# Optimization experiments

Measured on AMD Instinct MI355X. Metric: run time of the kernel, lower is better.

## Reference

```python
import jax, jax.numpy as jnp
import numpy as np

EPS = 1e-6


def _feature_map(x):
    # elu(x) + 1
    return jax.nn.elu(x) + 1.0


def _causal_dot(Qb, Kb, V):
    """Causal linear attention numerator for 3 stacked branches.
    Qb, Kb: [3, N, L, H, D]; V: [N, L, H, Dv] -> out [3, N, L, H, Dv].
    out[b,n,l,h,:] = sum_{s<=l} (Qb[b,n,l,h,:] . Kb[b,n,s,h,:]) V[n,s,h,:]
    computed with an O(L) recurrent scan over cumulative KV outer products.
    """
    Qs = jnp.moveaxis(Qb, 2, 0)  # [L, 3, N, H, D]
    Ks = jnp.moveaxis(Kb, 2, 0)  # [L, 3, N, H, D]
    Vs = jnp.moveaxis(V, 1, 0)   # [L, N, H, Dv]
    B, N, _, H, D = Qb.shape
    Dv = V.shape[-1]
    S0 = jnp.zeros((B, N, H, D, Dv), dtype=Qb.dtype)

    def step(S, inp):
        q, k, v = inp  # q,k: [3,N,H,D], v: [N,H,Dv]
        S = S + k[..., :, None] * v[None, :, :, None, :]
        o = jnp.einsum('bnhi,bnhij->bnhj', q, S)
        return S, o

    _, out = jax.lax.scan(step, S0, (Qs, Ks, Vs))  # out: [L,3,N,H,Dv]
    return jnp.moveaxis(out, 0, 2)  # [3,N,L,H,Dv]


def setup_inputs() -> dict:
    key = jax.random.key(0)
    ks = jax.random.split(key, 5)
    N, L, H, D = 4, 2048, 8, 128
    return {
        'queries': jax.random.normal(ks[0], (N, L, H, D), dtype=jnp.float32),
        'q2': jax.random.normal(ks[1], (N, L, H, D), dtype=jnp.float32),
        'keys': jax.random.normal(ks[2], (N, L, H, D), dtype=jnp.float32),
        'values': jax.random.normal(ks[3], (N, L, H, D), dtype=jnp.float32),
        'key_lengths': jnp.ones((N, L), dtype=jnp.float32),
        'omega': jax.random.normal(ks[4], (H, D, D), dtype=jnp.float32),
    }


def reference(queries, q2, keys, values, key_lengths, omega):
    N, L, H, D = queries.shape
    Q = _feature_map(queries)                       # [N,L,H,D]
    K = _feature_map(keys) * key_lengths[:, :, None, None]

    # Delta[n,l,h,i] = l/L for all n,h,i -> projection through omega reduces to
    # (l/L) * sum_i omega[h,i,j], same math as einsum('nlhi,hij->nlhj', Delta, omega).
    delta = (jnp.arange(L, dtype=queries.dtype) / L)        # [L]
    t = delta[:, None, None] * jnp.sum(omega, axis=1)[None]  # [L,H,D]
    sin_t, cos_t = jnp.sin(t), jnp.cos(t)
    s2, c2, sc = sin_t ** 2, cos_t ** 2, sin_t * cos_t       # [L,H,D] each

    # Q_term = sin(phi(q2))^2 * feature_map(queries)
    q2_proj = jnp.einsum('nlhi,hij->nlhj', q2, omega)
    Q_term = (jnp.sin(q2_proj) ** 2) * Q                     # [N,L,H,D]

    # Branch trig weights: Q gets [sin^2, cos^2, sin*cos], K gets [cos^2, sin^2, sin*cos]
    wq = jnp.stack([s2, c2, sc])[:, None]  # [3,1,L,H,D]
    wk = jnp.stack([c2, s2, sc])[:, None]
    Qb = Q_term[None] * wq                 # [3,N,L,H,D]
    Kb = K[None] * wk                      # [3,N,L,H,D]

    # Denominator terms Z_b = <Q_b[l], cumsum_{s<=l} K_b[s]>
    Kcum = jnp.cumsum(Kb, axis=2)
    Z = jnp.einsum('bnlhi,bnlhi->bnlh', Qb, Kcum)   # [3,N,L,H]

    Vb = _causal_dot(Qb, Kb, values)                # [3,N,L,H,D]

    numerator = Vb[0] + Vb[1] - 2.0 * Vb[2]
    denominator = Z[0] + Z[1] - 2.0 * Z[2] + EPS
    return numerator / denominator[:, :, :, None]
```

## Files before the change

kernel.cpp:

```cpp
#include <hip/hip_runtime.h>


typedef float f32x4 __attribute__((ext_vector_type(4)));
typedef short s16x8 __attribute__((ext_vector_type(8)));
typedef short s16x4 __attribute__((ext_vector_type(4)));
typedef unsigned short u16;

static constexpr int    Ln   = 2048;
static constexpr size_t NHLD = (size_t)32 * 2048 * 128;
static constexpr size_t KSB  = (size_t)32 * 16 * 128;

__device__ __forceinline__ float b2f(u16 s) {
  union { unsigned u; float f; } x; x.u = ((unsigned)s) << 16; return x.f;
}
__device__ __forceinline__ u16 f2b(float f) {
  union { float f; unsigned u; } x; x.f = f;
  unsigned r = x.u + 0x7fffu + ((x.u >> 16) & 1u);
  return (u16)(r >> 16);
}
__device__ __forceinline__ s16x8 pack8(f32x4 a, f32x4 b) {
  s16x8 r;
  r[0] = (short)f2b(a[0]); r[1] = (short)f2b(a[1]); r[2] = (short)f2b(a[2]); r[3] = (short)f2b(a[3]);
  r[4] = (short)f2b(b[0]); r[5] = (short)f2b(b[1]); r[6] = (short)f2b(b[2]); r[7] = (short)f2b(b[3]);
  return r;
}

__global__ __launch_bounds__(256) void k_omega(const float* __restrict__ om,
                                               u16* __restrict__ wt, float* __restrict__ osum) {
  __shared__ alignas(16) u16 T[128][136];
  int h = blockIdx.x, t = threadIdx.x;
  for (int idx = t; idx < 128 * 32; idx += 256) {
    int i = idx >> 5, cs = (idx & 31) << 2;
    f32x4 vv = *(const f32x4*)(om + ((size_t)(h * 128 + i)) * 128 + cs);
    T[i][cs + 0] = f2b(vv[0]); T[i][cs + 1] = f2b(vv[1]);
    T[i][cs + 2] = f2b(vv[2]); T[i][cs + 3] = f2b(vv[3]);
  }
  if (t < 128) {
    float acc = 0.f;
    for (int i = 0; i < 128; i++) acc += om[((size_t)(h * 128 + i)) * 128 + t];
    osum[h * 128 + t] = acc;
  }
  __syncthreads();
  {
    int j = t >> 1, lh = (t & 1) << 6;
    s16x8* dst = (s16x8*)(wt + ((size_t)(h * 128 + j)) * 128 + lh);
    for (int u = 0; u < 8; u++) {
      s16x8 pv;
#pragma unroll
      for (int e = 0; e < 8; e++) pv[e] = (short)T[lh + u * 8 + e][j];
      dst[u] = pv;
    }
  }
}

__global__ __launch_bounds__(256) void k_kvfeat(const float* __restrict__ kg, const float* __restrict__ vg,
                                                const float* __restrict__ klg, const float* __restrict__ osum,
                                                u16* __restrict__ kb3, u16* __restrict__ kbt3,
                                                u16* __restrict__ vt) {
  __shared__ alignas(16) u16 Bu[4][16][142];
  int bid = blockIdx.x, t = threadIdx.x;
  int ls = bid & 127, h = (bid >> 7) & 7, n = bid >> 10;
  int l0 = ls << 4, nh = (n << 3) + h;
  const float invL = 1.0f / 2048.0f;
  for (int idx = t; idx < 512; idx += 256) {
    int rr = idx >> 5, cs = (idx & 31) << 2;
    int l = l0 + rr;
    size_t gb = (((size_t)(n * Ln + l) * 8 + h) << 7) + cs;
    f32x4 kv = *(const f32x4*)(kg + gb);
    f32x4 vv = *(const f32x4*)(vg + gb);
    f32x4 osv = *(const f32x4*)(osum + h * 128 + cs);
    float klv = klg[n * Ln + l];
    float tb = (float)l * invL;
    u16 r0[4], r1[4], r2[4], r3[4];
#pragma unroll
    for (int e = 0; e < 4; e++) {
      float kf = (kv[e] > 0.f ? kv[e] + 1.f : __expf(kv[e])) * klv;
      float tt = tb * osv[e];
      float s, c; __sincosf(tt, &s, &c);
      r0[e] = f2b(kf * c * c);
      r1[e] = f2b(kf * s * s);
      r2[e] = f2b(kf * s * c);
      r3[e] = f2b(vv[e]);
    }
    *(unsigned*)&Bu[0][rr][cs]     = (unsigned)r0[0] | ((unsigned)r0[1] << 16);
    *(unsigned*)&Bu[0][rr][cs + 2] = (unsigned)r0[2] | ((unsigned)r0[3] << 16);
    *(unsigned*)&Bu[1][rr][cs]     = (unsigned)r1[0] | ((unsigned)r1[1] << 16);
    *(unsigned*)&Bu[1][rr][cs + 2] = (unsigned)r1[2] | ((unsigned)r1[3] << 16);
    *(unsigned*)&Bu[2][rr][cs]     = (unsigned)r2[0] | ((unsigned)r2[1] << 16);
    *(unsigned*)&Bu[2][rr][cs + 2] = (unsigned)r2[2] | ((unsigned)r2[3] << 16);
    *(unsigned*)&Bu[3][rr][cs]     = (unsigned)r3[0] | ((unsigned)r3[1] << 16);
    *(unsigned*)&Bu[3][rr][cs + 2] = (unsigned)r3[2] | ((unsigned)r3[3] << 16);
    size_t nb = ((size_t)nh * Ln + l) * 128 + cs;
    s16x4 p0, p1, p2;
#pragma unroll
    for (int e = 0; e < 4; e++) { p0[e] = (short)r0[e]; p1[e] = (short)r1[e]; p2[e] = (short)r2[e]; }
    *(s16x4*)(kb3 + nb)            = p0;
    *(s16x4*)(kb3 + NHLD + nb)     = p1;
    *(s16x4*)(kb3 + 2 * NHLD + nb) = p2;
  }
  __syncthreads();
  for (int idx = t; idx < 1024; idx += 256) {
    int arr = idx >> 8, rem = idx & 255, i = rem >> 1, half = rem & 1;
    int rb = half << 3;
    s16x8 pv;
#pragma unroll
    for (int u = 0; u < 8; u++) pv[u] = (short)Bu[arr][rb + u][i];
    u16* dst; size_t db;
    if (arr < 3) { dst = kbt3; db = ((size_t)((arr * 32 + nh) * 128 + i)) * Ln + l0 + rb; }
    else         { dst = vt;   db = ((size_t)(nh * 128 + i)) * Ln + l0 + rb; }
    *(s16x8*)(dst + db) = pv;
  }
}

__global__ __launch_bounds__(512, 4) void p1a(const u16* __restrict__ vtg, const u16* __restrict__ kbt3,
                                              u16* __restrict__ sct, float* __restrict__ ksum) {
  __shared__ alignas(16) u16 B[128][136];
  int bid = blockIdx.x, t = threadIdx.x;
  int c = bid & 15, h = (bid >> 4) & 7, n = (bid >> 7) & 3, b = bid >> 9;
  int l0 = c << 7, nh = (n << 3) + h, bnh = b * 32 + nh;
  int lane = t & 63, quad = lane >> 4, nl = lane & 15, w = t >> 6;
  for (int idx = t; idx < 2048; idx += 512) {
    int i = idx >> 4, cs = (idx & 15) << 3;
    *(s16x8*)&B[i][cs] = *(const s16x8*)(kbt3 + ((size_t)(bnh * 128 + i)) * Ln + l0 + cs);
  }
  __syncthreads();
  f32x4 z4 = {0.f, 0.f, 0.f, 0.f};
  f32x4 acc[8];
#pragma unroll
  for (int i = 0; i < 8; i++) acc[i] = z4;
  int arow = (w << 4) + nl;
  for (int ks = 0; ks < 4; ks++) {
    int k0 = (ks << 5) + (quad << 3);
    s16x8 av = *(const s16x8*)(vtg + ((size_t)(nh * 128 + arow)) * Ln + l0 + k0);
#pragma unroll
    for (int ct = 0; ct < 8; ct++) {
      s16x8 bv = *(const s16x8*)&B[(ct << 4) + nl][k0];
      acc[ct] = __builtin_amdgcn_mfma_f32_16x16x32_bf16(av, bv, acc[ct], 0, 0, 0);
    }
  }
  if (t < 128) {
    float s = 0.f;
#pragma unroll 4
    for (int g = 0; g < 128; g += 8) {
      s16x8 v = *(const s16x8*)&B[t][g];
#pragma unroll
      for (int e = 0; e < 8; e++) s += b2f((u16)v[e]);
    }
    ksum[(size_t)(bnh * 16 + c) * 128 + t] = s;
  }
  __syncthreads();
  {
    int lbase = (w << 4) + (quad << 2);
#pragma unroll
    for (int ct = 0; ct < 8; ct++) {
      int i = (ct << 4) + nl;
#pragma unroll
      for (int r = 0; r < 4; r++) B[lbase + r][i] = f2b(acc[ct][r]);
    }
  }
  __syncthreads();
  size_t sbase = ((size_t)(bnh * 16 + c)) << 14;
  for (int idx = t; idx < 2048; idx += 512) {
    int jr = idx >> 4, g = (idx & 15) << 3;
    *(s16x8*)(sct + sbase + ((size_t)jr << 7) + g) = *(const s16x8*)&B[jr][g];
  }
}

__global__ __launch_bounds__(256) void p1b(u16* __restrict__ sct, float* __restrict__ ksum) {
  int bid = blockIdx.x, t = threadIdx.x;
  if (bid < 768) {
    int tid = bid * 256 + t;
    int bnh = tid >> 11, rem = tid & 2047;
    size_t base = ((size_t)bnh << 18) + ((size_t)rem << 3);
    float acc[8] = {0.f, 0.f, 0.f, 0.f, 0.f, 0.f, 0.f, 0.f};
    for (int c = 0; c < 16; c++) {
      size_t a = base + ((size_t)c << 14);
      s16x8 v = *(const s16x8*)(sct + a);
      s16x8 o;
#pragma unroll
      for (int e = 0; e < 8; e++) { o[e] = (short)f2b(acc[e]); acc[e] += b2f((u16)v[e]); }
      *(s16x8*)(sct + a) = o;
    }
  } else {
    int m2 = (bid - 768) * 256 + t;
    int i = m2 & 127, bnh = m2 >> 7;
    size_t base = (size_t)bnh * 2048 + i;
    float acc = 0.f;
    for (int c = 0; c < 16; c++) {
      size_t a = base + (size_t)c * 128;
      float v = ksum[a];
      ksum[a] = acc;
      acc += v;
    }
  }
}

__global__ __launch_bounds__(256, 2) void k_qfeat(const float* __restrict__ q2g, const float* __restrict__ qg,
                                                  const u16* __restrict__ wt, const float* __restrict__ osum,
                                                  const float* __restrict__ kspre,
                                                  u16* __restrict__ qb3, float* __restrict__ zintg) {
  __shared__ alignas(16) u16 B[128][136];
  __shared__ float osb[128];
  int bid = blockIdx.x, t = threadIdx.x;
  int m = bid & 31, h = (bid >> 5) & 7, n = bid >> 8;
  int l0 = m << 6, c = m >> 1, nh = (n << 3) + h;
  if (t < 128) osb[t] = osum[h * 128 + t];
  for (int idx = t; idx < 2048; idx += 256) {
    int j = idx >> 4, cs = (idx & 15) << 3;
    *(s16x8*)&B[j][cs] = *(const s16x8*)(wt + ((size_t)(h * 128 + j)) * 128 + cs);
  }
  __syncthreads();
  int lane = t & 63, quad = lane >> 4, nl = lane & 15, w = t >> 6;
  f32x4 z4 = {0.f, 0.f, 0.f, 0.f};
  f32x4 acc[8];
#pragma unroll
  for (int i = 0; i < 8; i++) acc[i] = z4;
  int arow = l0 + (w << 4) + nl;
  for (int ks = 0; ks < 4; ks++) {
    int k0 = (ks << 5) + (quad << 3);
    const float* ap = q2g + (((size_t)(n * Ln + arow) * 8 + h) << 7) + k0;
    s16x8 av = pack8(*(const f32x4*)ap, *(const f32x4*)(ap + 4));
#pragma unroll
    for (int ct = 0; ct < 8; ct++) {
      s16x8 bv = *(const s16x8*)&B[(ct << 4) + nl][k0];
      acc[ct] = __builtin_amdgcn_mfma_f32_16x16x32_bf16(av, bv, acc[ct], 0, 0, 0);
    }
  }
  __syncthreads();
  {
    int lbase = (w << 4) + (quad << 2);
#pragma unroll
    for (int ct = 0; ct < 8; ct++) {
      int j = (ct << 4) + nl;
#pragma unroll
      for (int r = 0; r < 4; r++) {
        float sp = __sinf(acc[ct][r]);
        B[lbase + r][j] = f2b(sp * sp);
      }
    }
  }
  __syncthreads();
  const float invL = 1.0f / 2048.0f;
  for (int idx = t; idx < 1024; idx += 256) {
    int l = idx >> 4, j0 = (idx & 15) << 3, gl = l0 + l;
    s16x8 s2v = *(const s16x8*)&B[l][j0];
    const float* qp = qg + (((size_t)(n * Ln + gl) * 8 + h) << 7) + j0;
    f32x4 qa = *(const f32x4*)qp, qbv = *(const f32x4*)(qp + 4);
    size_t kbb = ((size_t)nh * 16 + c) * 128 + j0;
    f32x4 kp0a = *(const f32x4*)(kspre + kbb),           kp0b = *(const f32x4*)(kspre + kbb + 4);
    f32x4 kp1a = *(const f32x4*)(kspre + kbb + KSB),     kp1b = *(const f32x4*)(kspre + kbb + KSB + 4);
    f32x4 kp2a = *(const f32x4*)(kspre + kbb + 2 * KSB), kp2b = *(const f32x4*)(kspre + kbb + 2 * KSB + 4);
    s16x8 o0, o1, o2;
    float z = 0.f;
    float tb = (float)gl * invL;
#pragma unroll
    for (int e = 0; e < 8; e++) {
      float s2p = b2f((u16)s2v[e]);
      float qv = (e < 4) ? qa[e] : qbv[e - 4];
      float f = qv > 0.f ? qv + 1.f : __expf(qv);
      float Qt = s2p * f;
      float tt = tb * osb[j0 + e];
      float s, cc; __sincosf(tt, &s, &cc);
      float v0 = Qt * s * s, v1 = Qt * cc * cc, v2 = -2.f * Qt * s * cc;
      float k0v = (e < 4) ? kp0a[e] : kp0b[e - 4];
      float k1v = (e < 4) ? kp1a[e] : kp1b[e - 4];
      float k2v = (e < 4) ? kp2a[e] : kp2b[e - 4];
      z += v0 * k0v + v1 * k1v + v2 * k2v;
      o0[e] = (short)f2b(v0); o1[e] = (short)f2b(v1); o2[e] = (short)f2b(v2);
    }
    size_t base = ((size_t)nh * Ln + gl) * 128 + j0;
    *(s16x8*)(qb3 + base)            = o0;
    *(s16x8*)(qb3 + base + NHLD)     = o1;
    *(s16x8*)(qb3 + base + 2 * NHLD) = o2;
    z += __shfl_xor(z, 1); z += __shfl_xor(z, 2);
    z += __shfl_xor(z, 4); z += __shfl_xor(z, 8);
    if (nl == 0) zintg[(size_t)nh * Ln + gl] = z;
  }
}

__global__ __launch_bounds__(512, 4) void p3(const u16* __restrict__ qb3, const u16* __restrict__ kb3,
                                             const u16* __restrict__ vtg, const u16* __restrict__ sct,
                                             const float* __restrict__ zintg, float* __restrict__ outg) {
  __shared__ union {
    struct { alignas(16) u16 T0[128][136]; alignas(16) u16 T1[128][136]; } s;
    alignas(16) float O[128][132];
  } sm;
  int bid = blockIdx.x, t = threadIdx.x;
  int c = bid & 15, h = (bid >> 4) & 7, n = bid >> 7;
  int l0c = c << 7, nh = (n << 3) + h;
  int lane = t & 63, quad = lane >> 4, nl = lane & 15, w = t >> 6;
  f32x4 z4 = {0.f, 0.f, 0.f, 0.f};
  f32x4 accP[8], accO[8];
#pragma unroll
  for (int i = 0; i < 8; i++) { accP[i] = z4; accO[i] = z4; }
  int arow = l0c + (w << 4) + nl;
  for (int b = 0; b < 3; b++) {
    int bnh = b * 32 + nh;
    __syncthreads();
    for (int idx = t; idx < 2048; idx += 512) {
      int s = idx >> 4, cs = (idx & 15) << 3;
      *(s16x8*)&sm.s.T0[s][cs] = *(const s16x8*)(kb3 + (((size_t)bnh * Ln + l0c + s) << 7) + cs);
    }
    size_t sbase = ((size_t)(bnh * 16 + c)) << 14;
    for (int idx = t; idx < 2048; idx += 512) {
      int j = idx >> 4, cs = (idx & 15) << 3;
      *(s16x8*)&sm.s.T1[j][cs] = *(const s16x8*)(sct + sbase + ((size_t)j << 7) + cs);
    }
    __syncthreads();
    s16x8 av[4];
#pragma unroll
    for (int ks = 0; ks < 4; ks++)
      av[ks] = *(const s16x8*)(qb3 + (((size_t)bnh * Ln + arow) << 7) + (ks << 5) + (quad << 3));
    for (int ks = 0; ks < 4; ks++) {
      int k0 = (ks << 5) + (quad << 3);
#pragma unroll
      for (int ct = 0; ct < 8; ct++) {
        s16x8 bv0 = *(const s16x8*)&sm.s.T0[(ct << 4) + nl][k0];
        accP[ct] = __builtin_amdgcn_mfma_f32_16x16x32_bf16(av[ks], bv0, accP[ct], 0, 0, 0);
        s16x8 bv1 = *(const s16x8*)&sm.s.T1[(ct << 4) + nl][k0];
        accO[ct] = __builtin_amdgcn_mfma_f32_16x16x32_bf16(av[ks], bv1, accO[ct], 0, 0, 0);
      }
    }
  }
  __syncthreads();
  float zP[4] = {0.f, 0.f, 0.f, 0.f};
  int lbase = (w << 4) + (quad << 2);
#pragma unroll
  for (int ct = 0; ct < 8; ct++) {
    int ss = (ct << 4) + nl;
#pragma unroll
    for (int r = 0; r < 4; r++) {
      int lr = lbase + r;
      float pv = (ss <= lr) ? accP[ct][r] : 0.f;
      zP[r] += pv;
      sm.s.T0[lr][ss] = f2b(pv);
    }
  }
#pragma unroll
  for (int mteam = 1; mteam <= 8; mteam <<= 1) {
#pragma unroll
    for (int r = 0; r < 4; r++) zP[r] += __shfl_xor(zP[r], mteam);
  }
  for (int idx = t; idx < 2048; idx += 512) {
    int j = idx >> 4, cs = (idx & 15) << 3;
    *(s16x8*)&sm.s.T1[j][cs] = *(const s16x8*)(vtg + ((size_t)(nh * 128 + j)) * Ln + l0c + cs);
  }
  float zf[4];
#pragma unroll
  for (int r = 0; r < 4; r++)
    zf[r] = zintg[(size_t)nh * Ln + l0c + lbase + r] + zP[r] + 1e-6f;
  __syncthreads();
  for (int ks = 0; ks < 4; ks++) {
    int k0 = (ks << 5) + (quad << 3);
    s16x8 pav = *(const s16x8*)&sm.s.T0[(w << 4) + nl][k0];
#pragma unroll
    for (int ct = 0; ct < 8; ct++) {
      s16x8 vv = *(const s16x8*)&sm.s.T1[(ct << 4) + nl][k0];
      accO[ct] = __builtin_amdgcn_mfma_f32_16x16x32_bf16(pav, vv, accO[ct], 0, 0, 0);
    }
  }
  __syncthreads();
#pragma unroll
  for (int ct = 0; ct < 8; ct++) {
    int j = (ct << 4) + nl;
#pragma unroll
    for (int r = 0; r < 4; r++) sm.O[lbase + r][j] = accO[ct][r] / zf[r];
  }
  __syncthreads();
  for (int idx = t; idx < 4096; idx += 512) {
    int l = idx >> 5, g = (idx & 31) << 2;
    *(f32x4*)(outg + (((size_t)(n * Ln + l0c + l) * 8 + h) << 7) + g) = *(const f32x4*)&sm.O[l][g];
  }
}

extern "C" void kernel_launch(void* const* d_in, const int* in_sizes, int n_in,
                              void* d_out, int out_size, void* d_ws, size_t ws_size,
                              hipStream_t stream) {
  (void)in_sizes; (void)n_in; (void)out_size; (void)ws_size;
  const float* q   = (const float*)d_in[0];
  const float* q2  = (const float*)d_in[1];
  const float* kk  = (const float*)d_in[2];
  const float* vv  = (const float*)d_in[3];
  const float* kl  = (const float*)d_in[4];
  const float* om  = (const float*)d_in[5];
  float* out = (float*)d_out;

  u16* W     = (u16*)d_ws;
  u16* qb3   = W;
  u16* kb3   = W + 3 * NHLD;
  u16* kbt3  = W + 6 * NHLD;
  u16* vt    = W + 9 * NHLD;
  u16* sct   = W + 10 * NHLD;
  u16* wt    = W + 13 * NHLD;
  float* ks  = (float*)(W + 13 * NHLD + 131072);
  float* osm = ks + 196608;
  float* zin = osm + 1024;

  k_omega <<<8,    256, 0, stream>>>(om, wt, osm);
  k_kvfeat<<<4096, 256, 0, stream>>>(kk, vv, kl, osm, kb3, kbt3, vt);
  p1a     <<<1536, 512, 0, stream>>>(vt, kbt3, sct, ks);
  p1b     <<<816,  256, 0, stream>>>(sct, ks);
  k_qfeat <<<1024, 256, 0, stream>>>(q2, q, wt, osm, ks, qb3, zin);
  p3      <<<512,  512, 0, stream>>>(qb3, kb3, vt, sct, zin, out);
}
```

Baseline: 291.3 us.

## Store transposed K/V in contiguous 128x128 chunk tiles with swizzled LDS transpose

The K/V feature kernel now handles 128-row chunks per block instead of 16-row slabs. It writes the transposed kbt3 and vt arrays as contiguous 128x128 tiles per (head, chunk), using an XOR-swizzled shared-memory transpose done in two passes to fit LDS. The consumers p1a and p3 load each tile as one contiguous 32KB block instead of strided rows, which should improve coalescing for the writes and the later reads. The trade-offs are fewer blocks in k_kvfeat (512 instead of 4096), higher register use from holding r2 across passes, and more LDS per block.

Result: faster. 277.6 us (-4.7%).

```diff
diff --git a/kernel.cpp b/kernel.cpp
--- a/kernel.cpp
+++ b/kernel.cpp
@@ -57,58 +57,94 @@
                                                 const float* __restrict__ klg, const float* __restrict__ osum,
                                                 u16* __restrict__ kb3, u16* __restrict__ kbt3,
                                                 u16* __restrict__ vt) {
-  __shared__ alignas(16) u16 Bu[4][16][142];
+  __shared__ alignas(16) u16 T0[128][128], T1[128][128];
   int bid = blockIdx.x, t = threadIdx.x;
-  int ls = bid & 127, h = (bid >> 7) & 7, n = bid >> 10;
-  int l0 = ls << 4, nh = (n << 3) + h;
+  int c = bid & 15, h = (bid >> 4) & 7, n = bid >> 7;
+  int l0 = c << 7, nh = (n << 3) + h;
   const float invL = 1.0f / 2048.0f;
-  for (int idx = t; idx < 512; idx += 256) {
-    int rr = idx >> 5, cs = (idx & 31) << 2;
+  unsigned r2p[16][2];
+
+#pragma unroll
+  for (int it = 0; it < 16; it++) {
+    int idx = (it << 8) + t;
+    int rr = idx >> 5, g = idx & 31, cs = g << 2;
     int l = l0 + rr;
     size_t gb = (((size_t)(n * Ln + l) * 8 + h) << 7) + cs;
     f32x4 kv = *(const f32x4*)(kg + gb);
-    f32x4 vv = *(const f32x4*)(vg + gb);
     f32x4 osv = *(const f32x4*)(osum + h * 128 + cs);
     float klv = klg[n * Ln + l];
     float tb = (float)l * invL;
-    u16 r0[4], r1[4], r2[4], r3[4];
+    u16 r0[4], r1[4], r2[4];
 #pragma unroll
     for (int e = 0; e < 4; e++) {
       float kf = (kv[e] > 0.f ? kv[e] + 1.f : __expf(kv[e])) * klv;
       float tt = tb * osv[e];
-      float s, c; __sincosf(tt, &s, &c);
-      r0[e] = f2b(kf * c * c);
+      float s, cc; __sincosf(tt, &s, &cc);
+      r0[e] = f2b(kf * cc * cc);
       r1[e] = f2b(kf * s * s);
-      r2[e] = f2b(kf * s * c);
-      r3[e] = f2b(vv[e]);
-    }
-    *(unsigned*)&Bu[0][rr][cs]     = (unsigned)r0[0] | ((unsigned)r0[1] << 16);
-    *(unsigned*)&Bu[0][rr][cs + 2] = (unsigned)r0[2] | ((unsigned)r0[3] << 16);
-    *(unsigned*)&Bu[1][rr][cs]     = (unsigned)r1[0] | ((unsigned)r1[1] << 16);
-    *(unsigned*)&Bu[1][rr][cs + 2] = (unsigned)r1[2] | ((unsigned)r1[3] << 16);
-    *(unsigned*)&Bu[2][rr][cs]     = (unsigned)r2[0] | ((unsigned)r2[1] << 16);
-    *(unsigned*)&Bu[2][rr][cs + 2] = (unsigned)r2[2] | ((unsigned)r2[3] << 16);
-    *(unsigned*)&Bu[3][rr][cs]     = (unsigned)r3[0] | ((unsigned)r3[1] << 16);
-    *(unsigned*)&Bu[3][rr][cs + 2] = (unsigned)r3[2] | ((unsigned)r3[3] << 16);
+      r2[e] = f2b(kf * s * cc);
+    }
+    r2p[it][0] = (unsigned)r2[0] | ((unsigned)r2[1] << 16);
+    r2p[it][1] = (unsigned)r2[2] | ((unsigned)r2[3] << 16);
+    int gs = (g ^ (rr >> 3)) << 2;
+    *(s16x4*)&T0[rr][gs] = (s16x4){(short)r0[0], (short)r0[1], (short)r0[2], (short)r0[3]};
+    *(s16x4*)&T1[rr][gs] = (s16x4){(short)r1[0], (short)r1[1], (short)r1[2], (short)r1[3]};
     size_t nb = ((size_t)nh * Ln + l) * 128 + cs;
-    s16x4 p0, p1, p2;
-#pragma unroll
-    for (int e = 0; e < 4; e++) { p0[e] = (short)r0[e]; p1[e] = (short)r1[e]; p2[e] = (short)r2[e]; }
-    *(s16x4*)(kb3 + nb)            = p0;
-    *(s16x4*)(kb3 + NHLD + nb)     = p1;
-    *(s16x4*)(kb3 + 2 * NHLD + nb) = p2;
-  }
-  __syncthreads();
-  for (int idx = t; idx < 1024; idx += 256) {
-    int arr = idx >> 8, rem = idx & 255, i = rem >> 1, half = rem & 1;
-    int rb = half << 3;
-    s16x8 pv;
-#pragma unroll
-    for (int u = 0; u < 8; u++) pv[u] = (short)Bu[arr][rb + u][i];
-    u16* dst; size_t db;
-    if (arr < 3) { dst = kbt3; db = ((size_t)((arr * 32 + nh) * 128 + i)) * Ln + l0 + rb; }
-    else         { dst = vt;   db = ((size_t)(nh * 128 + i)) * Ln + l0 + rb; }
-    *(s16x8*)(dst + db) = pv;
+    *(s16x4*)(kb3 + nb)          = (s16x4){(short)r0[0], (short)r0[1], (short)r0[2], (short)r0[3]};
+    *(s16x4*)(kb3 + NHLD + nb)   = (s16x4){(short)r1[0], (short)r1[1], (short)r1[2], (short)r1[3]};
+    *(s16x4*)(kb3 + 2*NHLD + nb) = (s16x4){(short)r2[0], (short)r2[1], (short)r2[2], (short)r2[3]};
+  }
+  __syncthreads();
+  {
+    size_t b0 = ((size_t)(nh * 16 + c)) << 14;
+    size_t b1 = ((size_t)((32 + nh) * 16 + c)) << 14;
+    for (int idx = t; idx < 2048; idx += 256) {
+      int i = idx >> 4, o = idx & 15;
+      int gp = (((i >> 2) ^ o) << 2) + (i & 3);
+      s16x8 v0, v1;
+#pragma unroll
+      for (int u = 0; u < 8; u++) {
+        int r = (o << 3) + u;
+        v0[u] = (short)T0[r][gp];
+        v1[u] = (short)T1[r][gp];
+      }
+      size_t off = (((size_t)i) << 7) + (o << 3);
+      *(s16x8*)(kbt3 + b0 + off) = v0;
+      *(s16x8*)(kbt3 + b1 + off) = v1;
+    }
+  }
+  __syncthreads();
+#pragma unroll
+  for (int it = 0; it < 16; it++) {
+    int idx = (it << 8) + t;
+    int rr = idx >> 5, g = idx & 31, cs = g << 2;
+    int l = l0 + rr;
+    size_t gb = (((size_t)(n * Ln + l) * 8 + h) << 7) + cs;
+    f32x4 vv = *(const f32x4*)(vg + gb);
+    int gs = (g ^ (rr >> 3)) << 2;
+    *(s16x4*)&T1[rr][gs] = (s16x4){(short)f2b(vv[0]), (short)f2b(vv[1]),
+                                   (short)f2b(vv[2]), (short)f2b(vv[3])};
+    *(unsigned*)&T0[rr][gs]     = r2p[it][0];
+    *(unsigned*)&T0[rr][gs + 2] = r2p[it][1];
+  }
+  __syncthreads();
+  {
+    size_t b2 = ((size_t)((64 + nh) * 16 + c)) << 14;
+    size_t bv = ((size_t)(nh * 16 + c)) << 14;
+    for (int idx = t; idx < 2048; idx += 256) {
+      int i = idx >> 4, o = idx & 15;
+      int gp = (((i >> 2) ^ o) << 2) + (i & 3);
+      s16x8 v0, v1;
+#pragma unroll
+      for (int u = 0; u < 8; u++) {
+        int r = (o << 3) + u;
+        v0[u] = (short)T0[r][gp];
+        v1[u] = (short)T1[r][gp];
+      }
+      size_t off = (((size_t)i) << 7) + (o << 3);
+      *(s16x8*)(kbt3 + b2 + off) = v0;
+      *(s16x8*)(vt   + bv + off) = v1;
+    }
   }
 }
 
@@ -117,11 +153,11 @@
   __shared__ alignas(16) u16 B[128][136];
   int bid = blockIdx.x, t = threadIdx.x;
   int c = bid & 15, h = (bid >> 4) & 7, n = (bid >> 7) & 3, b = bid >> 9;
-  int l0 = c << 7, nh = (n << 3) + h, bnh = b * 32 + nh;
+  int nh = (n << 3) + h, bnh = b * 32 + nh;
   int lane = t & 63, quad = lane >> 4, nl = lane & 15, w = t >> 6;
+  size_t tbase = ((size_t)(bnh * 16 + c)) << 14;
   for (int idx = t; idx < 2048; idx += 512) {
-    int i = idx >> 4, cs = (idx & 15) << 3;
-    *(s16x8*)&B[i][cs] = *(const s16x8*)(kbt3 + ((size_t)(bnh * 128 + i)) * Ln + l0 + cs);
+    *(s16x8*)&B[idx >> 4][(idx & 15) << 3] = *(const s16x8*)(kbt3 + tbase + ((size_t)idx << 3));
   }
   __syncthreads();
   f32x4 z4 = {0.f, 0.f, 0.f, 0.f};
@@ -129,9 +165,10 @@
 #pragma unroll
   for (int i = 0; i < 8; i++) acc[i] = z4;
   int arow = (w << 4) + nl;
+  size_t vbase = ((size_t)(nh * 16 + c)) << 14;
   for (int ks = 0; ks < 4; ks++) {
     int k0 = (ks << 5) + (quad << 3);
-    s16x8 av = *(const s16x8*)(vtg + ((size_t)(nh * 128 + arow)) * Ln + l0 + k0);
+    s16x8 av = *(const s16x8*)(vtg + vbase + ((size_t)arow << 7) + k0);
 #pragma unroll
     for (int ct = 0; ct < 8; ct++) {
       s16x8 bv = *(const s16x8*)&B[(ct << 4) + nl][k0];
@@ -341,9 +378,9 @@
 #pragma unroll
     for (int r = 0; r < 4; r++) zP[r] += __shfl_xor(zP[r], mteam);
   }
+  size_t vbase = ((size_t)(nh * 16 + c)) << 14;
   for (int idx = t; idx < 2048; idx += 512) {
-    int j = idx >> 4, cs = (idx & 15) << 3;
-    *(s16x8*)&sm.s.T1[j][cs] = *(const s16x8*)(vtg + ((size_t)(nh * 128 + j)) * Ln + l0c + cs);
+    *(s16x8*)&sm.s.T1[idx >> 4][(idx & 15) << 3] = *(const s16x8*)(vtg + vbase + ((size_t)idx << 3));
   }
   float zf[4];
 #pragma unroll
@@ -397,7 +434,7 @@
   float* zin = osm + 1024;
 
   k_omega <<<8,    256, 0, stream>>>(om, wt, osm);
-  k_kvfeat<<<4096, 256, 0, stream>>>(kk, vv, kl, osm, kb3, kbt3, vt);
+  k_kvfeat<<<512,  256, 0, stream>>>(kk, vv, kl, osm, kb3, kbt3, vt);
   p1a     <<<1536, 512, 0, stream>>>(vt, kbt3, sct, ks);
   p1b     <<<816,  256, 0, stream>>>(sct, ks);
   k_qfeat <<<1024, 256, 0, stream>>>(q2, q, wt, osm, ks, qb3, zin);
```
